# Performance work log

Hardware: AMD Instinct MI355X
Metric: run time of the kernel (lower is better)

## Reference

```python
import jax, jax.numpy as jnp
import numpy as np

B, T, D, H = 4096, 512, 25, 25
NUM_LAYERS = 3


def setup_inputs() -> dict:
    key = jax.random.key(0)
    ks = jax.random.split(key, 9)
    s = 1.0 / np.sqrt(H)  # torch LSTM/Linear default init scale
    return {
        "x": jax.random.normal(ks[0], (B, T, D), dtype=jnp.float32),
        "Wih": jax.random.uniform(ks[1], (NUM_LAYERS, 4 * H, D), minval=-s, maxval=s),
        "Whh": jax.random.uniform(ks[2], (NUM_LAYERS, 4 * H, H), minval=-s, maxval=s),
        "bih": jax.random.uniform(ks[3], (NUM_LAYERS, 4 * H), minval=-s, maxval=s),
        "bhh": jax.random.uniform(ks[4], (NUM_LAYERS, 4 * H), minval=-s, maxval=s),
        "W1": jax.random.uniform(ks[5], (16, H), minval=-s, maxval=s),
        "b1": jax.random.uniform(ks[6], (16,), minval=-s, maxval=s),
        "W2": jax.random.uniform(ks[7], (14, 16), minval=-0.25, maxval=0.25),
        "b2": jax.random.uniform(ks[8], (14,), minval=-0.25, maxval=0.25),
    }


def _lstm_layer(x, Wih, Whh, b):
    """Single LSTM layer, batch_first. x: [B,T,Din] -> hs: [B,T,H].
    Torch gate order: i, f, g, o."""
    # Precompute input contribution for all timesteps at once: [B,T,4H]
    xg = jnp.einsum('btd,gd->btg', x, Wih) + b

    def step(carry, xg_t):
        h, c = carry
        g = xg_t + h @ Whh.T  # [B,4H]
        i, f, gg, o = jnp.split(g, 4, axis=-1)
        c = jax.nn.sigmoid(f) * c + jax.nn.sigmoid(i) * jnp.tanh(gg)
        h = jax.nn.sigmoid(o) * jnp.tanh(c)
        return (h, c), h

    h0 = jnp.zeros((x.shape[0], H), x.dtype)
    (_, _), hs = jax.lax.scan(step, (h0, h0), jnp.swapaxes(xg, 0, 1))  # [T,B,H]
    return jnp.swapaxes(hs, 0, 1)


def reference(x, Wih, Whh, bih, bhh, W1, b1, W2, b2):
    h = x
    for l in range(NUM_LAYERS):  # eval mode: inter-layer dropout disabled
        h = _lstm_layer(h, Wih[l], Whh[l], bih[l] + bhh[l])
    last = h[:, -1, :]                       # [B,H]
    out = jax.nn.relu(last @ W1.T + b1)      # [B,16]
    return jax.nn.softmax(out @ W2.T + b2, axis=1)  # [B,14]
```

## Files before the change

### kernel.cpp

```cpp
#include <hip/hip_runtime.h>


#define NBATCH 4096
#define NT     512
#define ND     25
#define NG     100
#define NL     3

__device__ __forceinline__ float sigf(float x) {
    return __builtin_amdgcn_rcpf(1.0f + __expf(-x));
}

__global__ __launch_bounds__(256)
void lstm_fused(const float* __restrict__ xin,
                const float* __restrict__ Wih,
                const float* __restrict__ Whh,
                const float* __restrict__ bih,
                const float* __restrict__ bhh,
                const float* __restrict__ W1,
                const float* __restrict__ b1,
                const float* __restrict__ W2,
                const float* __restrict__ b2,
                float* __restrict__ out,
                float* __restrict__ ws)
{
    __shared__ __align__(16) float xs[4][32];
    __shared__ __align__(16) float hs[4][32];

    const int wid  = threadIdx.x >> 6;
    const int lane = threadIdx.x & 63;
    const int b    = (blockIdx.x << 2) + wid;

    const int row0 = lane;
    int row1 = 64 + lane; if (row1 > 99) row1 = 99;

    float wih0[25], whh0[25], wih1[25], whh1[25];

    if (lane < 32) { xs[wid][lane] = 0.f; hs[wid][lane] = 0.f; }

    for (int l = 0; l < NL; ++l) {
        const float* wihp0 = Wih + (l*NG + row0)*ND;
        const float* whhp0 = Whh + (l*NG + row0)*ND;
        const float* wihp1 = Wih + (l*NG + row1)*ND;
        const float* whhp1 = Whh + (l*NG + row1)*ND;
#pragma unroll
        for (int d = 0; d < 25; ++d) {
            wih0[d] = wihp0[d]; whh0[d] = whhp0[d];
            wih1[d] = wihp1[d]; whh1[d] = whhp1[d];
        }
        const float bias0 = bih[l*NG + row0] + bhh[l*NG + row0];
        const float bias1 = bih[l*NG + row1] + bhh[l*NG + row1];

        float c = 0.f;
        if (lane < 32) hs[wid][lane] = 0.f;

        const float* src = (l == 0) ? (xin + (size_t)b * NT * ND)
                                    : (ws  + (size_t)b * NT * ND);
        float* wsrow = ws + (size_t)b * NT * ND;

        float xv_next = (lane < 25) ? src[lane] : 0.f;

        for (int t = 0; t < NT; ++t) {
            if (lane < 25) {
                xs[wid][lane] = xv_next;
                if (t + 1 < NT) xv_next = src[(t + 1) * ND + lane];
            }

            float acc0 = bias0, acc1 = bias1;
#pragma unroll
            for (int c4 = 0; c4 < 7; ++c4) {
                const float4 xv = *(const float4*)&xs[wid][c4 * 4];
                const float4 hv = *(const float4*)&hs[wid][c4 * 4];
                const float xa[4] = {xv.x, xv.y, xv.z, xv.w};
                const float ha[4] = {hv.x, hv.y, hv.z, hv.w};
#pragma unroll
                for (int j = 0; j < 4; ++j) {
                    const int d = c4 * 4 + j;
                    if (d < 25) {
                        acc0 = fmaf(wih0[d], xa[j], acc0);
                        acc1 = fmaf(wih1[d], xa[j], acc1);
                        acc0 = fmaf(whh0[d], ha[j], acc0);
                        acc1 = fmaf(whh1[d], ha[j], acc1);
                    }
                }
            }

            const float in0 = (lane < 50) ? acc0 : acc0 + acc0;
            const float s0  = sigf(in0);
            const float act0 = (lane < 50) ? s0 : s0 + s0 - 1.0f;
            const float in1 = (lane < 11) ? acc1 + acc1 : acc1;
            const float s1  = sigf(in1);
            const float act1 = (lane < 11) ? s1 + s1 - 1.0f : s1;

            const float fg = __shfl(act0, (lane + 25) & 63);
            const float ga = __shfl(act0, (lane + 50) & 63);
            const float gb = __shfl(act1, (lane + 50) & 63);
            const float og = __shfl(act1, (lane + 11) & 63);
            const float gg = (lane < 14) ? ga : gb;
            const float ig = act0;

            c = fmaf(fg, c, ig * gg);
            float th = sigf(c + c); th = th + th - 1.0f;
            const float hnew = og * th;

            if (lane < 25) {
                hs[wid][lane] = hnew;
                if (l < 2) wsrow[t * ND + lane] = hnew;
            }
        }
    }

    if (lane < 16) {
        float u = b1[lane];
#pragma unroll
        for (int d = 0; d < 25; ++d) u = fmaf(W1[lane * 25 + d], hs[wid][d], u);
        xs[wid][lane] = fmaxf(u, 0.f);
    }
    if (lane < 14) {
        float lg = b2[lane];
#pragma unroll
        for (int r = 0; r < 16; ++r) lg = fmaf(W2[lane * 16 + r], xs[wid][r], lg);
        hs[wid][lane] = lg;
    }
    if (lane < 14) {
        float m = -1e30f;
#pragma unroll
        for (int j = 0; j < 14; ++j) m = fmaxf(m, hs[wid][j]);
        float sum = 0.f;
#pragma unroll
        for (int j = 0; j < 14; ++j) sum += __expf(hs[wid][j] - m);
        const float lg = hs[wid][lane];
        out[b * 14 + lane] = __expf(lg - m) / sum;
    }
}

extern "C" void kernel_launch(void* const* d_in, const int* in_sizes, int n_in,
                              void* d_out, int out_size, void* d_ws, size_t ws_size,
                              hipStream_t stream)
{
    const float* x   = (const float*)d_in[0];
    const float* Wih = (const float*)d_in[1];
    const float* Whh = (const float*)d_in[2];
    const float* bih = (const float*)d_in[3];
    const float* bhh = (const float*)d_in[4];
    const float* W1  = (const float*)d_in[5];
    const float* b1  = (const float*)d_in[6];
    const float* W2  = (const float*)d_in[7];
    const float* b2  = (const float*)d_in[8];
    float* outp = (float*)d_out;
    float* ws   = (float*)d_ws;

    dim3 grid(NBATCH / 4), block(256);
    hipLaunchKernelGGL(lstm_fused, grid, block, 0, stream,
                       x, Wih, Whh, bih, bhh, W1, b1, W2, b2, outp, ws);
}
```

Before: 1.971 ms.

## Split LSTM gate rows across two cooperating waves per batch element

Each batch element is now handled by two wavefronts instead of one. Each lane computes a single gate row over a combined 50-element [x;h] vector held in shared memory, rather than two rows per lane exchanged with shuffles. Gate activations go through LDS, and one updater wave computes c and h. The intent is to shorten the per-step FMA chain per wave and raise occupancy by doubling the block count, with launch bounds set to 4. The cost is two block-wide barriers per timestep and an extra LDS round trip for the activations.

New measurement: 1.884 ms. -4.4%, faster.

```diff
diff --git a/kernel.cpp b/kernel.cpp
--- a/kernel.cpp
+++ b/kernel.cpp
@@ -10,127 +10,113 @@
 __device__ __forceinline__ float sigf(float x) {
     return __builtin_amdgcn_rcpf(1.0f + __expf(-x));
 }
+__device__ __forceinline__ float tanhfast(float x) {
+    float s = sigf(x + x);
+    return s + s - 1.0f;
+}
 
-__global__ __launch_bounds__(256)
-void lstm_fused(const float* __restrict__ xin,
-                const float* __restrict__ Wih,
-                const float* __restrict__ Whh,
-                const float* __restrict__ bih,
-                const float* __restrict__ bhh,
-                const float* __restrict__ W1,
-                const float* __restrict__ b1,
-                const float* __restrict__ W2,
-                const float* __restrict__ b2,
-                float* __restrict__ out,
-                float* __restrict__ ws)
+__global__ __launch_bounds__(256, 4)
+void lstm2(const float* __restrict__ xin,
+           const float* __restrict__ Wih,
+           const float* __restrict__ Whh,
+           const float* __restrict__ bih,
+           const float* __restrict__ bhh,
+           const float* __restrict__ W1,
+           const float* __restrict__ b1,
+           const float* __restrict__ W2,
+           const float* __restrict__ b2,
+           float* __restrict__ out,
+           float* __restrict__ ws)
 {
-    __shared__ __align__(16) float xs[4][32];
-    __shared__ __align__(16) float hs[4][32];
+    __shared__ __align__(16) float xh[2][56];
+    __shared__ float act[2][112];
 
     const int wid  = threadIdx.x >> 6;
     const int lane = threadIdx.x & 63;
-    const int b    = (blockIdx.x << 2) + wid;
+    const int wb   = wid >> 1;
+    const int role = wid & 1;
+    const int b    = (blockIdx.x << 1) + wb;
 
-    const int row0 = lane;
-    int row1 = 64 + lane; if (row1 > 99) row1 = 99;
+    const int  lrow    = (lane < 50) ? lane : 49;
+    const bool updater = (role == 0) && (lane < 25);
 
-    float wih0[25], whh0[25], wih1[25], whh1[25];
-
-    if (lane < 32) { xs[wid][lane] = 0.f; hs[wid][lane] = 0.f; }
+    float w[52];
+    w[50] = 0.f; w[51] = 0.f;
 
     for (int l = 0; l < NL; ++l) {
-        const float* wihp0 = Wih + (l*NG + row0)*ND;
-        const float* whhp0 = Whh + (l*NG + row0)*ND;
-        const float* wihp1 = Wih + (l*NG + row1)*ND;
-        const float* whhp1 = Whh + (l*NG + row1)*ND;
+        const int row = l * NG + role * 50 + lrow;
+        const float* wihp = Wih + row * ND;
+        const float* whhp = Whh + row * ND;
 #pragma unroll
-        for (int d = 0; d < 25; ++d) {
-            wih0[d] = wihp0[d]; whh0[d] = whhp0[d];
-            wih1[d] = wihp1[d]; whh1[d] = whhp1[d];
-        }
-        const float bias0 = bih[l*NG + row0] + bhh[l*NG + row0];
-        const float bias1 = bih[l*NG + row1] + bhh[l*NG + row1];
-
-        float c = 0.f;
-        if (lane < 32) hs[wid][lane] = 0.f;
+        for (int d = 0; d < 25; ++d) { w[d] = wihp[d]; w[25 + d] = whhp[d]; }
+        const float bias = bih[row] + bhh[row];
 
         const float* src = (l == 0) ? (xin + (size_t)b * NT * ND)
                                     : (ws  + (size_t)b * NT * ND);
         float* wsrow = ws + (size_t)b * NT * ND;
 
-        float xv_next = (lane < 25) ? src[lane] : 0.f;
+        float c = 0.f;
+        float xv_next = 0.f;
+        if (updater) {
+            xh[wb][lane] = src[lane];
+            xv_next = src[ND + lane];
+        }
+        if (role == 0 && lane < 31) xh[wb][25 + lane] = 0.f;
+        __syncthreads();
 
         for (int t = 0; t < NT; ++t) {
-            if (lane < 25) {
-                xs[wid][lane] = xv_next;
-                if (t + 1 < NT) xv_next = src[(t + 1) * ND + lane];
+            float acc = bias;
+#pragma unroll
+            for (int c4 = 0; c4 < 13; ++c4) {
+                const float4 v = *(const float4*)&xh[wb][c4 * 4];
+                acc = fmaf(w[c4 * 4 + 0], v.x, acc);
+                acc = fmaf(w[c4 * 4 + 1], v.y, acc);
+                acc = fmaf(w[c4 * 4 + 2], v.z, acc);
+                acc = fmaf(w[c4 * 4 + 3], v.w, acc);
             }
+            float a;
+            if (role == 0) a = sigf(acc);
+            else           a = (lane < 25) ? tanhfast(acc)
+                                           : sigf(acc);
+            if (lane < 50) act[wb][role * 56 + lane] = a;
+            __syncthreads();
 
-            float acc0 = bias0, acc1 = bias1;
-#pragma unroll
-            for (int c4 = 0; c4 < 7; ++c4) {
-                const float4 xv = *(const float4*)&xs[wid][c4 * 4];
-                const float4 hv = *(const float4*)&hs[wid][c4 * 4];
-                const float xa[4] = {xv.x, xv.y, xv.z, xv.w};
-                const float ha[4] = {hv.x, hv.y, hv.z, hv.w};
-#pragma unroll
-                for (int j = 0; j < 4; ++j) {
-                    const int d = c4 * 4 + j;
-                    if (d < 25) {
-                        acc0 = fmaf(wih0[d], xa[j], acc0);
-                        acc1 = fmaf(wih1[d], xa[j], acc1);
-                        acc0 = fmaf(whh0[d], ha[j], acc0);
-                        acc1 = fmaf(whh1[d], ha[j], acc1);
-                    }
-                }
+            if (updater) {
+                const float ig = act[wb][lane];
+                const float fg = act[wb][25 + lane];
+                const float gg = act[wb][56 + lane];
+                const float og = act[wb][81 + lane];
+                c = fmaf(fg, c, ig * gg);
+                const float h = og * tanhfast(c);
+                xh[wb][25 + lane] = h;
+                xh[wb][lane]      = xv_next;
+                if (l < 2) wsrow[t * ND + lane] = h;
+                if (t + 2 < NT) xv_next = src[(t + 2) * ND + lane];
             }
-
-            const float in0 = (lane < 50) ? acc0 : acc0 + acc0;
-            const float s0  = sigf(in0);
-            const float act0 = (lane < 50) ? s0 : s0 + s0 - 1.0f;
-            const float in1 = (lane < 11) ? acc1 + acc1 : acc1;
-            const float s1  = sigf(in1);
-            const float act1 = (lane < 11) ? s1 + s1 - 1.0f : s1;
-
-            const float fg = __shfl(act0, (lane + 25) & 63);
-            const float ga = __shfl(act0, (lane + 50) & 63);
-            const float gb = __shfl(act1, (lane + 50) & 63);
-            const float og = __shfl(act1, (lane + 11) & 63);
-            const float gg = (lane < 14) ? ga : gb;
-            const float ig = act0;
-
-            c = fmaf(fg, c, ig * gg);
-            float th = sigf(c + c); th = th + th - 1.0f;
-            const float hnew = og * th;
-
-            if (lane < 25) {
-                hs[wid][lane] = hnew;
-                if (l < 2) wsrow[t * ND + lane] = hnew;
-            }
+            __syncthreads();
         }
     }
 
-    if (lane < 16) {
+    if (role == 0 && lane < 16) {
         float u = b1[lane];
 #pragma unroll
-        for (int d = 0; d < 25; ++d) u = fmaf(W1[lane * 25 + d], hs[wid][d], u);
-        xs[wid][lane] = fmaxf(u, 0.f);
+        for (int d = 0; d < 25; ++d) u = fmaf(W1[lane * 25 + d], xh[wb][25 + d], u);
+        act[wb][lane] = fmaxf(u, 0.f);
     }
-    if (lane < 14) {
+    if (role == 0 && lane < 14) {
         float lg = b2[lane];
 #pragma unroll
-        for (int r = 0; r < 16; ++r) lg = fmaf(W2[lane * 16 + r], xs[wid][r], lg);
-        hs[wid][lane] = lg;
+        for (int r = 0; r < 16; ++r) lg = fmaf(W2[lane * 16 + r], act[wb][r], lg);
+        act[wb][32 + lane] = lg;
     }
-    if (lane < 14) {
+    if (role == 0 && lane < 14) {
         float m = -1e30f;
 #pragma unroll
-        for (int j = 0; j < 14; ++j) m = fmaxf(m, hs[wid][j]);
+        for (int j = 0; j < 14; ++j) m = fmaxf(m, act[wb][32 + j]);
         float sum = 0.f;
 #pragma unroll
-        for (int j = 0; j < 14; ++j) sum += __expf(hs[wid][j] - m);
-        const float lg = hs[wid][lane];
-        out[b * 14 + lane] = __expf(lg - m) / sum;
+        for (int j = 0; j < 14; ++j) sum += __expf(act[wb][32 + j] - m);
+        out[b * 14 + lane] = __expf(act[wb][32 + lane] - m) / sum;
     }
 }
 
@@ -150,7 +136,7 @@
     float* outp = (float*)d_out;
     float* ws   = (float*)d_ws;
 
-    dim3 grid(NBATCH / 4), block(256);
-    hipLaunchKernelGGL(lstm_fused, grid, block, 0, stream,
+    dim3 grid(NBATCH / 2), block(256);
+    hipLaunchKernelGGL(lstm2, grid, block, 0, stream,
                        x, Wih, Whh, bih, bhh, W1, b1, W2, b2, outp, ws);
 }
```
